# Performance work log

Measured on AMD Instinct MI355X. Metric: run time of the kernel, lower is better.

## Reference

```python
import jax, jax.numpy as jnp
import numpy as np

EPS = 1e-8
QMAX = 127.0


def _quantize_per_token(x):
    # x: (B, S, H) -> int8-valued floats and per-token scale (B, S, 1)
    amax = jnp.clip(jnp.max(jnp.abs(x), axis=-1, keepdims=True), EPS, None)
    scale = amax / QMAX
    x_q = jnp.clip(jnp.round(x / scale), -128.0, 127.0)
    return x_q.astype(jnp.int8), scale


def _quantize_per_channel(w):
    # w: (O, I) -> int8-valued and per-output-channel scale (O, 1)
    amax = jnp.clip(jnp.max(jnp.abs(w), axis=-1, keepdims=True), EPS, None)
    scale = amax / QMAX
    w_q = jnp.clip(jnp.round(w / scale), -128.0, 127.0)
    return w_q.astype(jnp.int8), scale


def setup_inputs() -> dict:
    key = jax.random.key(0)
    k1, k2, k3 = jax.random.split(key, 3)
    B, S, I, O = 4, 2048, 4096, 4096
    x = jax.random.normal(k1, (B, S, I), dtype=jnp.float32)
    weight = jax.random.normal(k2, (O, I), dtype=jnp.float32) * 0.02
    bias = jax.random.normal(k3, (O,), dtype=jnp.float32) * 0.01
    return {"x": x, "weight": weight, "bias": bias}


def reference(x, weight, bias):
    # Prequantized weight (done once at init in the original module)
    w_int8, w_scale = _quantize_per_channel(weight)  # (O, I), (O, 1)
    # Per-token input quantization
    x_int8, x_scale = _quantize_per_token(x)          # (B, S, I), (B, S, 1)
    # int8 GEMM with int32 accumulate, then dequant
    out_i32 = jnp.einsum(
        "bsi,oi->bso",
        x_int8.astype(jnp.int32),
        w_int8.astype(jnp.int32),
    )
    out = out_i32.astype(jnp.float32) * x_scale * w_scale.T  # (B,S,O)*(B,S,1)*(1,O)
    out = out + bias
    return out.astype(x.dtype)
```

## Files before the change

### kernel.cpp

```cpp
#include <hip/hip_runtime.h>

using i32x4 = __attribute__((ext_vector_type(4))) int;

#define QMAXF 127.0f
#define EPSF 1e-8f

__device__ __forceinline__ void gload_lds16(const void* g, void* l) {
    __builtin_amdgcn_global_load_lds(
        (const __attribute__((address_space(1))) void*)g,
        (__attribute__((address_space(3))) void*)l,
        16, 0, 0);
}

__global__ __launch_bounds__(256) void quant_rows_kernel(
    const float* __restrict__ in, signed char* __restrict__ q,
    float* __restrict__ scale, int K) {
    const int row = blockIdx.x;
    const int t = threadIdx.x;
    const float4* rp = reinterpret_cast<const float4*>(in + (size_t)row * K);

    float4 v[4];
#pragma unroll
    for (int j = 0; j < 4; ++j) v[j] = rp[j * 256 + t];

    float amax = 0.f;
#pragma unroll
    for (int j = 0; j < 4; ++j) {
        amax = fmaxf(amax, fabsf(v[j].x));
        amax = fmaxf(amax, fabsf(v[j].y));
        amax = fmaxf(amax, fabsf(v[j].z));
        amax = fmaxf(amax, fabsf(v[j].w));
    }
#pragma unroll
    for (int off = 32; off > 0; off >>= 1)
        amax = fmaxf(amax, __shfl_xor(amax, off));

    __shared__ float red[4];
    if ((t & 63) == 0) red[t >> 6] = amax;
    __syncthreads();
    amax = fmaxf(fmaxf(red[0], red[1]), fmaxf(red[2], red[3]));
    amax = fmaxf(amax, EPSF);
    const float s = amax / QMAXF;
    if (t == 0) scale[row] = s;

    int* qrow = reinterpret_cast<int*>(q + (size_t)row * K);
#pragma unroll
    for (int j = 0; j < 4; ++j) {
        const int b0 = (int)fminf(fmaxf(rintf(v[j].x / s), -128.f), 127.f);
        const int b1 = (int)fminf(fmaxf(rintf(v[j].y / s), -128.f), 127.f);
        const int b2 = (int)fminf(fmaxf(rintf(v[j].z / s), -128.f), 127.f);
        const int b3 = (int)fminf(fmaxf(rintf(v[j].w / s), -128.f), 127.f);
        qrow[j * 256 + t] =
            (b0 & 255) | ((b1 & 255) << 8) | ((b2 & 255) << 16) | ((b3 & 255) << 24);
    }
}

#define BM 128
#define BN 128
#define BKB 128

__global__ __launch_bounds__(256, 3) void int8_gemm_kernel(
    const signed char* __restrict__ A,
    const signed char* __restrict__ B,
    const float* __restrict__ xscale,
    const float* __restrict__ wscale,
    const float* __restrict__ bias,
    float* __restrict__ out,
    int M, int N, int K) {
    __shared__ signed char sA[BM * BKB];
    __shared__ signed char sB[BN * BKB];

    const int t = threadIdx.x;

    const int nwg = gridDim.x;
    const int cpx = nwg >> 3;
    const int swz = (blockIdx.x & 7) * cpx + (blockIdx.x >> 3);
    const int tilesN = N / BN;
    const size_t m0 = (size_t)(swz / tilesN) * BM;
    const size_t n0 = (size_t)(swz % tilesN) * BN;

    const signed char* aSrc[4];
    const signed char* bSrc[4];
    int ldst[4];
#pragma unroll
    for (int p = 0; p < 4; ++p) {
        const int o = p * 4096 + t * 16;
        const int row = o >> 7;
        const int slot = (o >> 4) & 7;
        const int gcol = (slot ^ (row & 7)) << 4;
        ldst[p] = o;
        aSrc[p] = A + (m0 + row) * (size_t)K + gcol;
        bSrc[p] = B + (n0 + row) * (size_t)K + gcol;
    }

    const int lane = t & 63;
    const int l15 = lane & 15;
    const int lhi = lane >> 4;
    const int l7 = lane & 7;
    const int wv = t >> 6;
    const int wr = wv >> 1;
    const int wc = wv & 1;

    int aoff[2][4], boff[2][4];
#pragma unroll
    for (int kk = 0; kk < 2; ++kk)
#pragma unroll
        for (int i = 0; i < 4; ++i) {
            const int slot = ((kk << 2) | lhi) ^ l7;
            aoff[kk][i] = (wr * 64 + i * 16 + l15) * BKB + (slot << 4);
            boff[kk][i] = (wc * 64 + i * 16 + l15) * BKB + (slot << 4);
        }

    i32x4 acc[4][4];
    const i32x4 zero = {0, 0, 0, 0};
#pragma unroll
    for (int i = 0; i < 4; ++i)
#pragma unroll
        for (int j = 0; j < 4; ++j) acc[i][j] = zero;

    const int ksteps = K / BKB;
    for (int kt = 0; kt < ksteps; ++kt) {
#pragma unroll
        for (int p = 0; p < 4; ++p) {
            gload_lds16(aSrc[p], sA + ldst[p]);
            gload_lds16(bSrc[p], sB + ldst[p]);
        }
#pragma unroll
        for (int p = 0; p < 4; ++p) { aSrc[p] += BKB; bSrc[p] += BKB; }
        __syncthreads();
#pragma unroll
        for (int kk = 0; kk < 2; ++kk) {
            i32x4 af[4], bf[4];
#pragma unroll
            for (int i = 0; i < 4; ++i)
                af[i] = *reinterpret_cast<const i32x4*>(sA + aoff[kk][i]);
#pragma unroll
            for (int j = 0; j < 4; ++j)
                bf[j] = *reinterpret_cast<const i32x4*>(sB + boff[kk][j]);
#pragma unroll
            for (int i = 0; i < 4; ++i)
#pragma unroll
                for (int j = 0; j < 4; ++j)
                    acc[i][j] = __builtin_amdgcn_mfma_i32_16x16x64_i8(
                        af[i], bf[j], acc[i][j], 0, 0, 0);
        }
        __syncthreads();
    }

#pragma unroll
    for (int i = 0; i < 4; ++i) {
        float xs[4];
#pragma unroll
        for (int r = 0; r < 4; ++r)
            xs[r] = xscale[m0 + wr * 64 + i * 16 + lhi * 4 + r];
#pragma unroll
        for (int j = 0; j < 4; ++j) {
            const int n = (int)n0 + wc * 64 + j * 16 + l15;
            const float wsv = wscale[n];
            const float bv = bias[n];
#pragma unroll
            for (int r = 0; r < 4; ++r) {
                const size_t m = m0 + wr * 64 + i * 16 + lhi * 4 + r;
                out[m * (size_t)N + n] = ((float)acc[i][j][r] * xs[r]) * wsv + bv;
            }
        }
    }
}

extern "C" void kernel_launch(void* const* d_in, const int* in_sizes, int n_in,
                              void* d_out, int out_size, void* d_ws, size_t ws_size,
                              hipStream_t stream) {
    const float* x = (const float*)d_in[0];
    const float* w = (const float*)d_in[1];
    const float* bias = (const float*)d_in[2];
    float* out = (float*)d_out;

    const int O = in_sizes[2];
    const int I = in_sizes[1] / O;
    const int M = in_sizes[0] / I;

    char* ws = (char*)d_ws;
    signed char* xq = (signed char*)ws;
    signed char* wq = xq + (size_t)M * I;
    float* xs = (float*)(wq + (size_t)O * I);
    float* wsc = xs + M;

    quant_rows_kernel<<<M, 256, 0, stream>>>(x, xq, xs, I);
    quant_rows_kernel<<<O, 256, 0, stream>>>(w, wq, wsc, I);

    const int grid = (M / BM) * (O / BN);
    int8_gemm_kernel<<<grid, 256, 0, stream>>>(xq, wq, xs, wsc, bias, out,
                                               M, O, I);
}
```

Measured before the change: 415.6 us.

## Triple-buffer LDS with async prefetch and enlarge GEMM tile to 256x128 with 8 waves

The GEMM kernel now keeps three LDS stages and issues global-to-LDS loads two k-tiles ahead. Explicit vmcnt waits and raw barriers replace the load-then-sync loop, so memory latency can overlap MFMA work. The block tile grows to 256x128 with 512 threads, which halves how often B tiles are re-read per output. MFMA sections also get raised wave priority. The cost is 144KB of LDS per block and two blocks per CU at most, so occupancy drops.

Measured after the change: 423.2 us. Within noise of the previous version (+1.8%).

```diff
diff --git a/kernel.cpp b/kernel.cpp
--- a/kernel.cpp
+++ b/kernel.cpp
@@ -55,11 +55,15 @@
     }
 }
 
-#define BM 128
+#define BM 256
 #define BN 128
 #define BKB 128
-
-__global__ __launch_bounds__(256, 3) void int8_gemm_kernel(
+#define NBUF 3
+#define ABYTES (BM * BKB)
+#define BBYTES (BN * BKB)
+#define BUFSZ (ABYTES + BBYTES)
+
+__global__ __launch_bounds__(512, 2) void int8_gemm_kernel(
     const signed char* __restrict__ A,
     const signed char* __restrict__ B,
     const float* __restrict__ xscale,
@@ -67,8 +71,7 @@
     const float* __restrict__ bias,
     float* __restrict__ out,
     int M, int N, int K) {
-    __shared__ signed char sA[BM * BKB];
-    __shared__ signed char sB[BN * BKB];
+    __shared__ signed char sAB[NBUF * BUFSZ];
 
     const int t = threadIdx.x;
 
@@ -80,16 +83,25 @@
     const size_t n0 = (size_t)(swz % tilesN) * BN;
 
     const signed char* aSrc[4];
-    const signed char* bSrc[4];
-    int ldst[4];
+    int aDst[4];
+    const signed char* bSrc[2];
+    int bDst[2];
 #pragma unroll
     for (int p = 0; p < 4; ++p) {
-        const int o = p * 4096 + t * 16;
+        const int o = p * 8192 + t * 16;
         const int row = o >> 7;
         const int slot = (o >> 4) & 7;
         const int gcol = (slot ^ (row & 7)) << 4;
-        ldst[p] = o;
+        aDst[p] = o;
         aSrc[p] = A + (m0 + row) * (size_t)K + gcol;
+    }
+#pragma unroll
+    for (int p = 0; p < 2; ++p) {
+        const int o = p * 8192 + t * 16;
+        const int row = o >> 7;
+        const int slot = (o >> 4) & 7;
+        const int gcol = (slot ^ (row & 7)) << 4;
+        bDst[p] = ABYTES + o;
         bSrc[p] = B + (n0 + row) * (size_t)K + gcol;
     }
 
@@ -98,17 +110,17 @@
     const int lhi = lane >> 4;
     const int l7 = lane & 7;
     const int wv = t >> 6;
-    const int wr = wv >> 1;
-    const int wc = wv & 1;
+    const int wvm = wv >> 1;
+    const int wvn = wv & 1;
 
     int aoff[2][4], boff[2][4];
 #pragma unroll
     for (int kk = 0; kk < 2; ++kk)
 #pragma unroll
-        for (int i = 0; i < 4; ++i) {
+        for (int f = 0; f < 4; ++f) {
             const int slot = ((kk << 2) | lhi) ^ l7;
-            aoff[kk][i] = (wr * 64 + i * 16 + l15) * BKB + (slot << 4);
-            boff[kk][i] = (wc * 64 + i * 16 + l15) * BKB + (slot << 4);
+            aoff[kk][f] = (wvm * 64 + f * 16 + l15) * BKB + (slot << 4);
+            boff[kk][f] = ABYTES + (wvn * 64 + f * 16 + l15) * BKB + (slot << 4);
         }
 
     i32x4 acc[4][4];
@@ -118,50 +130,78 @@
 #pragma unroll
         for (int j = 0; j < 4; ++j) acc[i][j] = zero;
 
-    const int ksteps = K / BKB;
-    for (int kt = 0; kt < ksteps; ++kt) {
-#pragma unroll
-        for (int p = 0; p < 4; ++p) {
-            gload_lds16(aSrc[p], sA + ldst[p]);
-            gload_lds16(bSrc[p], sB + ldst[p]);
-        }
-#pragma unroll
-        for (int p = 0; p < 4; ++p) { aSrc[p] += BKB; bSrc[p] += BKB; }
-        __syncthreads();
+    const int nt = K / BKB;
+
+#pragma unroll
+    for (int p = 0; p < 4; ++p) gload_lds16(aSrc[p], sAB + aDst[p]);
+#pragma unroll
+    for (int p = 0; p < 2; ++p) gload_lds16(bSrc[p], sAB + bDst[p]);
+#pragma unroll
+    for (int p = 0; p < 4; ++p) gload_lds16(aSrc[p] + BKB, sAB + BUFSZ + aDst[p]);
+#pragma unroll
+    for (int p = 0; p < 2; ++p) gload_lds16(bSrc[p] + BKB, sAB + BUFSZ + bDst[p]);
+
+    int cbuf = 0;
+    int sbuf = 2;
+    for (int kt = 0; kt < nt; ++kt) {
+        if (kt + 2 < nt) {
+            const size_t ko = (size_t)(kt + 2) * BKB;
+            const int sb = sbuf * BUFSZ;
+#pragma unroll
+            for (int p = 0; p < 4; ++p) gload_lds16(aSrc[p] + ko, sAB + sb + aDst[p]);
+#pragma unroll
+            for (int p = 0; p < 2; ++p) gload_lds16(bSrc[p] + ko, sAB + sb + bDst[p]);
+        }
+        if (kt < nt - 2)
+            asm volatile("s_waitcnt vmcnt(12)" ::: "memory");
+        else if (kt == nt - 2)
+            asm volatile("s_waitcnt vmcnt(6)" ::: "memory");
+        else
+            asm volatile("s_waitcnt vmcnt(0)" ::: "memory");
+        __builtin_amdgcn_s_barrier();
+        asm volatile("" ::: "memory");
+
+        const signed char* base = sAB + cbuf * BUFSZ;
 #pragma unroll
         for (int kk = 0; kk < 2; ++kk) {
             i32x4 af[4], bf[4];
 #pragma unroll
-            for (int i = 0; i < 4; ++i)
-                af[i] = *reinterpret_cast<const i32x4*>(sA + aoff[kk][i]);
-#pragma unroll
-            for (int j = 0; j < 4; ++j)
-                bf[j] = *reinterpret_cast<const i32x4*>(sB + boff[kk][j]);
+            for (int f = 0; f < 4; ++f)
+                af[f] = *reinterpret_cast<const i32x4*>(base + aoff[kk][f]);
+#pragma unroll
+            for (int f = 0; f < 4; ++f)
+                bf[f] = *reinterpret_cast<const i32x4*>(base + boff[kk][f]);
+            __builtin_amdgcn_s_setprio(1);
 #pragma unroll
             for (int i = 0; i < 4; ++i)
 #pragma unroll
                 for (int j = 0; j < 4; ++j)
                     acc[i][j] = __builtin_amdgcn_mfma_i32_16x16x64_i8(
                         af[i], bf[j], acc[i][j], 0, 0, 0);
-        }
-        __syncthreads();
-    }
-
-#pragma unroll
-    for (int i = 0; i < 4; ++i) {
-        float xs[4];
+            __builtin_amdgcn_s_setprio(0);
+        }
+
+        asm volatile("" ::: "memory");
+        __builtin_amdgcn_s_barrier();
+        cbuf = (cbuf == NBUF - 1) ? 0 : cbuf + 1;
+        sbuf = (sbuf == NBUF - 1) ? 0 : sbuf + 1;
+    }
+
+#pragma unroll
+    for (int f = 0; f < 4; ++f) {
+        float xsv[4];
 #pragma unroll
         for (int r = 0; r < 4; ++r)
-            xs[r] = xscale[m0 + wr * 64 + i * 16 + lhi * 4 + r];
-#pragma unroll
-        for (int j = 0; j < 4; ++j) {
-            const int n = (int)n0 + wc * 64 + j * 16 + l15;
+            xsv[r] = xscale[m0 + wvm * 64 + f * 16 + lhi * 4 + r];
+#pragma unroll
+        for (int g = 0; g < 4; ++g) {
+            const int n = (int)n0 + wvn * 64 + g * 16 + l15;
             const float wsv = wscale[n];
             const float bv = bias[n];
 #pragma unroll
             for (int r = 0; r < 4; ++r) {
-                const size_t m = m0 + wr * 64 + i * 16 + lhi * 4 + r;
-                out[m * (size_t)N + n] = ((float)acc[i][j][r] * xs[r]) * wsv + bv;
+                const size_t m = m0 + wvm * 64 + f * 16 + lhi * 4 + r;
+                out[m * (size_t)N + n] = ((float)acc[f][g][r] * xsv[r]) * wsv + bv;
             }
         }
     }
@@ -189,6 +229,6 @@
     quant_rows_kernel<<<O, 256, 0, stream>>>(w, wq, wsc, I);
 
     const int grid = (M / BM) * (O / BN);
-    int8_gemm_kernel<<<grid, 256, 0, stream>>>(xq, wq, xs, wsc, bias, out,
+    int8_gemm_kernel<<<grid, 512, 0, stream>>>(xq, wq, xs, wsc, bias, out,
                                                M, O, I);
 }
```
